# Kernel tuning notes

Hardware: AMD Instinct MI355X
Metric: run time of the kernel (lower is better)

Reference implementation:

```python
import jax, jax.numpy as jnp
import numpy as np

B, S, H = 1, 2048, 2048
I = 1408
E = 64
TOP_K = 8
N_GROUP = 8
TOPK_GROUP = 4
SCALE = 2.5
N_SHARED = 2


def setup_inputs() -> dict:
    key = jax.random.key(0)
    ks = jax.random.split(key, 9)
    x = jax.random.normal(ks[0], (B, S, H), dtype=jnp.float32)
    # kaiming_uniform(a=sqrt(5)) for [E, H] weight -> bound = 1/sqrt(H)
    gate_w = jax.random.uniform(ks[1], (E, H), jnp.float32, -1.0, 1.0) / jnp.sqrt(float(H))
    e_bias = jnp.zeros((E,), jnp.float32)
    gate_proj = jax.random.normal(ks[2], (E, I, H), jnp.float32) * 0.02
    up_proj = jax.random.normal(ks[3], (E, I, H), jnp.float32) * 0.02
    down_proj = jax.random.normal(ks[4], (E, H, I), jnp.float32) * 0.02
    SI = I * N_SHARED
    shared_gate_w = jax.random.uniform(ks[5], (SI, H), jnp.float32, -1.0, 1.0) / jnp.sqrt(float(H))
    shared_up_w = jax.random.uniform(ks[6], (SI, H), jnp.float32, -1.0, 1.0) / jnp.sqrt(float(H))
    shared_down_w = jax.random.uniform(ks[7], (H, SI), jnp.float32, -1.0, 1.0) / jnp.sqrt(float(SI))
    return {"hidden_states": x, "gate_w": gate_w, "e_bias": e_bias,
            "gate_proj": gate_proj, "up_proj": up_proj, "down_proj": down_proj,
            "shared_gate_w": shared_gate_w, "shared_up_w": shared_up_w,
            "shared_down_w": shared_down_w}


def _moe_forward(hidden_states, gate_w, e_bias, gate_proj, up_proj, down_proj,
                 shared_gate_w, shared_up_w, shared_down_w):
    bsz, seq_len, h = hidden_states.shape
    xf = hidden_states.reshape(-1, h).astype(jnp.float32)  # [T, H]
    T = bsz * seq_len

    # ---- DeepSeek group-restricted top-k gating ----
    logits = xf @ gate_w.T                                  # [T, E]
    scores = jax.nn.sigmoid(logits)
    scores_for_choice = scores + e_bias[None, :]
    gs = scores_for_choice.reshape(T, N_GROUP, E // N_GROUP)
    group_scores = jax.lax.top_k(gs, 2)[0].sum(-1)          # [T, n_group] sum of top-2 per group
    group_idx = jax.lax.top_k(group_scores, TOPK_GROUP)[1]  # [T, topk_group]
    group_mask = jax.nn.one_hot(group_idx, N_GROUP, dtype=jnp.float32).sum(1)  # [T, n_group]
    score_mask = jnp.repeat(group_mask, E // N_GROUP, axis=1)                  # [T, E]
    tmp_scores = jnp.where(score_mask > 0, scores_for_choice, 0.0)
    topk_idx = jax.lax.top_k(tmp_scores, TOP_K)[1]          # [T, top_k]
    topk_w = jnp.take_along_axis(scores, topk_idx, axis=1)  # gather from UN-biased scores
    topk_w = topk_w / (topk_w.sum(-1, keepdims=True) + 1e-20)
    topk_w = topk_w * SCALE

    # Dense combine weights [T, E]; exactly equivalent to sort/dispatch/combine.
    rows = jnp.arange(T)
    cw = jnp.zeros((T, E), jnp.float32).at[rows[:, None], topk_idx].add(topk_w)

    # ---- per-expert FFN, accumulated with lax.scan over the (fixed) expert axis ----
    def step(y, we):
        Wg, Wu, Wd, w = we                                  # [I,H],[I,H],[H,I],[T]
        g = xf @ Wg.T                                       # [T, I]
        u = xf @ Wu.T
        inter = jax.nn.silu(g) * u                          # silu_mul kernel
        out = inter @ Wd.T                                  # [T, H]
        return y + out * w[:, None], None

    y0 = jnp.zeros_like(xf)
    y, _ = jax.lax.scan(step, y0, (gate_proj, up_proj, down_proj, cw.T))
    y = y.reshape(bsz, seq_len, h)

    # ---- shared experts ----
    sg = hidden_states @ shared_gate_w.T                    # [B, S, SI]
    su = hidden_states @ shared_up_w.T
    shared_out = (jax.nn.silu(sg) * su) @ shared_down_w.T   # [B, S, H]
    return y + shared_out


def reference(hidden_states, gate_w, e_bias, gate_proj, up_proj, down_proj,
              shared_gate_w, shared_up_w, shared_down_w):
    return _moe_forward(hidden_states, gate_w, e_bias, gate_proj, up_proj, down_proj,
                        shared_gate_w, shared_up_w, shared_down_w)
```

## Files before the change

### kernel.cpp

```cpp
#include <hip/hip_runtime.h>

typedef unsigned short u16;
typedef unsigned int u32;
typedef __attribute__((ext_vector_type(8))) short short8;
typedef __attribute__((ext_vector_type(8))) u16 ushort8;
typedef __attribute__((ext_vector_type(4))) float f32x4;

#define T_TOK 2048
#define H_DIM 2048
#define NEXP 64
#define I_DIM 1408
#define SI_DIM 2816
#define BM 128
#define BK 64
#define MAXT 512

__device__ __forceinline__ u16 f2bf(float f) {
    u32 u = __builtin_bit_cast(u32, f);
    u32 r = u + 0x7FFFu + ((u >> 16) & 1u);
    return (u16)(r >> 16);
}

__device__ __forceinline__ ushort8 cvt8(f32x4 a, f32x4 b) {
    ushort8 o;
    o[0] = f2bf(a[0]); o[1] = f2bf(a[1]); o[2] = f2bf(a[2]); o[3] = f2bf(a[3]);
    o[4] = f2bf(b[0]); o[5] = f2bf(b[1]); o[6] = f2bf(b[2]); o[7] = f2bf(b[3]);
    return o;
}

__device__ __forceinline__ f32x4 mfma16(short8 a, short8 b, f32x4 c) {
    return __builtin_amdgcn_mfma_f32_16x16x32_bf16(a, b, c, 0, 0, 0);
}

__global__ __launch_bounds__(256) void k_cvt(const float* __restrict__ x, u16* __restrict__ xb) {
    int i = (blockIdx.x * 256 + threadIdx.x) * 8;
    f32x4 v0 = *(const f32x4*)(x + i);
    f32x4 v1 = *(const f32x4*)(x + i + 4);
    *(ushort8*)(xb + i) = cvt8(v0, v1);
}

__global__ __launch_bounds__(256) void k_gate_logits(const float* __restrict__ x,
        const float* __restrict__ gw, float* __restrict__ logits) {
    __shared__ float xs[8][65];
    __shared__ float wsh[64][65];
    int tid = threadIdx.x;
    int t0 = blockIdx.x * 8;
    double acc0 = 0.0, acc1 = 0.0;
    int e = tid & 63, tg = tid >> 6;
    for (int k0 = 0; k0 < H_DIM; k0 += 64) {
        #pragma unroll
        for (int s = 0; s < 2; ++s) {
            int idx = s * 256 + tid;
            int r = idx >> 6, k = idx & 63;
            xs[r][k] = x[(size_t)(t0 + r) * H_DIM + k0 + k];
        }
        #pragma unroll
        for (int s = 0; s < 16; ++s) {
            int idx = s * 256 + tid;
            int r = idx >> 6, k = idx & 63;
            wsh[r][k] = gw[(size_t)r * H_DIM + k0 + k];
        }
        __syncthreads();
        #pragma unroll 8
        for (int k = 0; k < 64; ++k) {
            double wv = (double)wsh[e][k];
            acc0 += (double)xs[tg][k] * wv;
            acc1 += (double)xs[tg + 4][k] * wv;
        }
        __syncthreads();
    }
    logits[(size_t)(t0 + tg) * NEXP + e] = (float)acc0;
    logits[(size_t)(t0 + tg + 4) * NEXP + e] = (float)acc1;
}

__global__ __launch_bounds__(256) void k_topk(const float* __restrict__ logits,
        const float* __restrict__ ebias, int* __restrict__ topk_idx,
        float* __restrict__ topk_w, int* __restrict__ counts) {
    __shared__ float bsh[64];
    if (threadIdx.x < 64) bsh[threadIdx.x] = ebias[threadIdx.x];
    __syncthreads();
    int t = blockIdx.x * 256 + threadIdx.x;
    float sc[64];
    #pragma unroll
    for (int e2 = 0; e2 < 64; ++e2) {
        float lg = logits[(size_t)t * 64 + e2];
        sc[e2] = 1.0f / (1.0f + expf(-lg));
    }
    float gsc[8];
    #pragma unroll
    for (int g = 0; g < 8; ++g) {
        float m1 = -1e30f, m2 = -1e30f;
        #pragma unroll
        for (int j = 0; j < 8; ++j) {
            float v = sc[g * 8 + j] + bsh[g * 8 + j];
            if (v > m1) { m2 = m1; m1 = v; }
            else if (v > m2) { m2 = v; }
        }
        gsc[g] = m1 + m2;
    }
    u32 gmask = 0;
    #pragma unroll
    for (int it = 0; it < 4; ++it) {
        float best = -1e30f; int bi = 0;
        #pragma unroll
        for (int g = 0; g < 8; ++g) {
            bool ok = !((gmask >> g) & 1u);
            if (ok && gsc[g] > best) { best = gsc[g]; bi = g; }
        }
        gmask |= 1u << bi;
    }
    unsigned long long avail = 0ull;
    #pragma unroll
    for (int g = 0; g < 8; ++g)
        if ((gmask >> g) & 1u) avail |= (0xFFull << (g * 8));
    float wsum = 0.f;
    int idx[8]; float wv[8];
    #pragma unroll
    for (int it = 0; it < 8; ++it) {
        float best = -1e30f, bw = 0.f; int bi = 0;
        #pragma unroll
        for (int e2 = 0; e2 < 64; ++e2) {
            bool ok = (avail >> e2) & 1ull;
            float v = sc[e2] + bsh[e2];
            if (ok && v > best) { best = v; bi = e2; bw = sc[e2]; }
        }
        avail &= ~(1ull << bi);
        idx[it] = bi; wv[it] = bw; wsum += bw;
    }
    float scale = 2.5f / (wsum + 1e-20f);
    #pragma unroll
    for (int it = 0; it < 8; ++it) {
        topk_idx[t * 8 + it] = idx[it];
        topk_w[t * 8 + it] = wv[it] * scale;
        atomicAdd(&counts[idx[it]], 1);
    }
}

__global__ void k_prefix(const int* __restrict__ counts, int* __restrict__ offsets,
                         int* __restrict__ tiles_gu, int* __restrict__ tiles_dn) {
    if (threadIdx.x == 0) {
        int run = 0;
        for (int e = 0; e < 64; ++e) { offsets[e] = run; run += counts[e]; }
        offsets[64] = run;
        for (int i = 0; i < MAXT; ++i) { tiles_gu[i] = -1; tiles_dn[i] = -1; }
        int sg[8] = {0,0,0,0,0,0,0,0};
        int sd[8] = {0,0,0,0,0,0,0,0};
        for (int j = 0; j < SI_DIM / 64; ++j) {
            int xcd = j & 7;
            int pos = xcd + 8 * sg[xcd];
            if (pos < MAXT) { tiles_gu[pos] = (64 << 16) | (j * 64); sg[xcd]++; }
        }
        for (int j = 0; j < H_DIM / 128; ++j) {
            int xcd = j & 7;
            int pos = xcd + 8 * sd[xcd];
            if (pos < MAXT) { tiles_dn[pos] = (64 << 16) | (j * 128); sd[xcd]++; }
        }
        for (int e = 0; e < 64; ++e) {
            int xcd = e & 7;
            int c = counts[e];
            for (int m0 = 0; m0 < c; m0 += BM) {
                int pg = xcd + 8 * sg[xcd];
                if (pg < MAXT) { tiles_gu[pg] = (e << 16) | m0; sg[xcd]++; }
                int pd = xcd + 8 * sd[xcd];
                if (pd < MAXT) { tiles_dn[pd] = (e << 16) | m0; sd[xcd]++; }
            }
        }
    }
}

__global__ __launch_bounds__(256) void k_scatter(const int* __restrict__ topk_idx,
        const float* __restrict__ topk_w, const int* __restrict__ offsets,
        int* __restrict__ fill, int* __restrict__ tok_list, float* __restrict__ w_list) {
    int gid = blockIdx.x * 256 + threadIdx.x;
    int t = gid >> 3;
    int e = topk_idx[gid];
    int pos = offsets[e] + atomicAdd(&fill[e], 1);
    tok_list[pos] = t;
    w_list[pos] = topk_w[gid];
}

__global__ __launch_bounds__(256, 2) void k_gateup(
        const u16* __restrict__ xb,
        const float* __restrict__ gr, const float* __restrict__ ur,
        const float* __restrict__ gs, const float* __restrict__ us,
        const int* __restrict__ offsets, const int* __restrict__ tok_list,
        const int* __restrict__ tiles,
        u16* __restrict__ inter_r, u16* __restrict__ inter_s) {
    int tt = tiles[blockIdx.x];
    if (tt < 0) return;
    int e = tt >> 16;
    const float *Bg, *Bu; u16* op; const int* tl;
    int m0, seg, n, i0, Irows;
    if (e < 64) {
        m0 = tt & 0xFFFF; seg = offsets[e]; n = offsets[e + 1] - seg;
        if (n <= 0 || m0 >= n) return;
        i0 = blockIdx.y * 64;
        Bg = gr + (size_t)e * I_DIM * H_DIM;
        Bu = ur + (size_t)e * I_DIM * H_DIM;
        op = inter_r; Irows = I_DIM; tl = tok_list;
    } else {
        if (blockIdx.y >= T_TOK / BM) return;
        i0 = tt & 0xFFFF; m0 = blockIdx.y * BM; seg = 0; n = T_TOK;
        Bg = gs; Bu = us;
        op = inter_s; Irows = SI_DIM; tl = nullptr;
    }

    __shared__ u16 As[2][BM * BK];
    __shared__ u16 Bsg[2][64 * BK];
    __shared__ u16 Bsu[2][64 * BK];

    int tid = threadIdx.x;
    int w = tid >> 6, lane = tid & 63;

    const u16* asrc[4]; int adst[4];
    #pragma unroll
    for (int s = 0; s < 4; ++s) {
        int slot = s * 256 + tid;
        int r = slot >> 3, cb = slot & 7;
        int p = m0 + r; if (p >= n) p = n - 1;
        int tok = tl ? tl[seg + p] : p;
        asrc[s] = xb + (size_t)tok * H_DIM + cb * 8;
        adst[s] = r * BK + ((cb ^ (r & 7)) * 8);
    }
    const float* bgsrc[2]; const float* busrc[2]; int bdst[2];
    #pragma unroll
    for (int s = 0; s < 2; ++s) {
        int slot = s * 256 + tid;
        int r = slot >> 3, cb = slot & 7;
        bgsrc[s] = Bg + (size_t)(i0 + r) * H_DIM + cb * 8;
        busrc[s] = Bu + (size_t)(i0 + r) * H_DIM + cb * 8;
        bdst[s] = r * BK + ((cb ^ (r & 7)) * 8);
    }

    f32x4 zero; zero[0] = 0.f; zero[1] = 0.f; zero[2] = 0.f; zero[3] = 0.f;
    f32x4 accg[2][4], accu[2][4];
    #pragma unroll
    for (int a = 0; a < 2; ++a)
        #pragma unroll
        for (int b = 0; b < 4; ++b) { accg[a][b] = zero; accu[a][b] = zero; }

    short8 stA0[4], stA1[4];
    f32x4 stG0[2][2], stU0[2][2], stG1[2][2], stU1[2][2];

    auto ldS0 = [&](int t) {
        int k0 = t * BK;
        #pragma unroll
        for (int s = 0; s < 4; ++s) stA0[s] = *(const short8*)(asrc[s] + k0);
        #pragma unroll
        for (int s = 0; s < 2; ++s) {
            stG0[s][0] = *(const f32x4*)(bgsrc[s] + k0);
            stG0[s][1] = *(const f32x4*)(bgsrc[s] + k0 + 4);
            stU0[s][0] = *(const f32x4*)(busrc[s] + k0);
            stU0[s][1] = *(const f32x4*)(busrc[s] + k0 + 4);
        }
    };
    auto ldS1 = [&](int t) {
        int k0 = t * BK;
        #pragma unroll
        for (int s = 0; s < 4; ++s) stA1[s] = *(const short8*)(asrc[s] + k0);
        #pragma unroll
        for (int s = 0; s < 2; ++s) {
            stG1[s][0] = *(const f32x4*)(bgsrc[s] + k0);
            stG1[s][1] = *(const f32x4*)(bgsrc[s] + k0 + 4);
            stU1[s][0] = *(const f32x4*)(busrc[s] + k0);
            stU1[s][1] = *(const f32x4*)(busrc[s] + k0 + 4);
        }
    };
    auto dsw0 = [&]() {
        #pragma unroll
        for (int s = 0; s < 4; ++s) *(ushort8*)(&As[0][adst[s]]) = *(const ushort8*)&stA0[s];
        #pragma unroll
        for (int s = 0; s < 2; ++s) {
            *(ushort8*)(&Bsg[0][bdst[s]]) = cvt8(stG0[s][0], stG0[s][1]);
            *(ushort8*)(&Bsu[0][bdst[s]]) = cvt8(stU0[s][0], stU0[s][1]);
        }
    };
    auto dsw1 = [&]() {
        #pragma unroll
        for (int s = 0; s < 4; ++s) *(ushort8*)(&As[1][adst[s]]) = *(const ushort8*)&stA1[s];
        #pragma unroll
        for (int s = 0; s < 2; ++s) {
            *(ushort8*)(&Bsg[1][bdst[s]]) = cvt8(stG1[s][0], stG1[s][1]);
            *(ushort8*)(&Bsu[1][bdst[s]]) = cvt8(stU1[s][0], stU1[s][1]);
        }
    };
    auto mmaStep = [&](int buf) {
        #pragma unroll
        for (int ks = 0; ks < 2; ++ks) {
            short8 a[2];
            #pragma unroll
            for (int fm = 0; fm < 2; ++fm) {
                int row = w * 32 + fm * 16 + (lane & 15);
                int cb = ks * 4 + (lane >> 4);
                a[fm] = *(const short8*)(&As[buf][row * BK + ((cb ^ (row & 7)) * 8)]);
            }
            #pragma unroll
            for (int fn = 0; fn < 4; ++fn) {
                int brow = fn * 16 + (lane & 15);
                int cb = ks * 4 + (lane >> 4);
                int boff = brow * BK + ((cb ^ (brow & 7)) * 8);
                short8 bg = *(const short8*)(&Bsg[buf][boff]);
                short8 bu = *(const short8*)(&Bsu[buf][boff]);
                accg[0][fn] = mfma16(a[0], bg, accg[0][fn]);
                accg[1][fn] = mfma16(a[1], bg, accg[1][fn]);
                accu[0][fn] = mfma16(a[0], bu, accu[0][fn]);
                accu[1][fn] = mfma16(a[1], bu, accu[1][fn]);
            }
        }
    };

    const int NK = H_DIM / BK;
    ldS0(0); dsw0();
    ldS1(1);
    __syncthreads();
    for (int t = 0; t < NK; t += 2) {
        if (t + 2 < NK) ldS0(t + 2);
        mmaStep(0);
        if (t + 1 < NK) dsw1();
        __syncthreads();
        if (t + 1 < NK) {
            if (t + 3 < NK) ldS1(t + 3);
            mmaStep(1);
            if (t + 2 < NK) dsw0();
            __syncthreads();
        }
    }

    int r0 = (lane >> 4) * 4, cc = lane & 15;
    #pragma unroll
    for (int fm = 0; fm < 2; ++fm) {
        #pragma unroll
        for (int r = 0; r < 4; ++r) {
            int p = m0 + w * 32 + fm * 16 + r0 + r;
            if (p < n) {
                size_t rowb = (size_t)(seg + p) * Irows + i0;
                #pragma unroll
                for (int fn = 0; fn < 4; ++fn) {
                    float g = accg[fm][fn][r], u = accu[fm][fn][r];
                    float val = g / (1.0f + expf(-g)) * u;
                    op[rowb + fn * 16 + cc] = f2bf(val);
                }
            }
        }
    }
}

__global__ __launch_bounds__(256, 2) void k_down(
        const u16* __restrict__ inter_r, const u16* __restrict__ inter_s,
        const float* __restrict__ dr, const float* __restrict__ dsw,
        const int* __restrict__ offsets, const int* __restrict__ tok_list,
        const int* __restrict__ tiles,
        const float* __restrict__ w_list,
        float* __restrict__ out) {
    int tt = tiles[blockIdx.x];
    if (tt < 0) return;
    int e = tt >> 16;
    const float* Bd; const u16* interp; const int* tl; const float* wl;
    int m0, seg, n, h0, Kdim;
    if (e < 64) {
        m0 = tt & 0xFFFF; seg = offsets[e]; n = offsets[e + 1] - seg;
        if (n <= 0 || m0 >= n) return;
        h0 = blockIdx.y * 128;
        Bd = dr + (size_t)e * H_DIM * I_DIM;
        interp = inter_r; Kdim = I_DIM; tl = tok_list; wl = w_list;
    } else {
        h0 = tt & 0xFFFF; m0 = blockIdx.y * BM; seg = 0; n = T_TOK;
        Bd = dsw; interp = inter_s; Kdim = SI_DIM; tl = nullptr; wl = nullptr;
    }

    __shared__ u16 As[2][BM * BK];
    __shared__ u16 Bs[2][128 * BK];

    int tid = threadIdx.x;
    int w = tid >> 6, lane = tid & 63;

    const u16* asrc[4]; int adst[4];
    #pragma unroll
    for (int s = 0; s < 4; ++s) {
        int slot = s * 256 + tid;
        int r = slot >> 3, cb = slot & 7;
        int p = m0 + r; if (p >= n) p = n - 1;
        asrc[s] = interp + (size_t)(seg + p) * Kdim + cb * 8;
        adst[s] = r * BK + ((cb ^ (r & 7)) * 8);
    }
    const float* bsrc[4]; int bdst[4];
    #pragma unroll
    for (int s = 0; s < 4; ++s) {
        int slot = s * 256 + tid;
        int r = slot >> 3, cb = slot & 7;
        bsrc[s] = Bd + (size_t)(h0 + r) * Kdim + cb * 8;
        bdst[s] = r * BK + ((cb ^ (r & 7)) * 8);
    }

    f32x4 zero; zero[0] = 0.f; zero[1] = 0.f; zero[2] = 0.f; zero[3] = 0.f;
    f32x4 acc[2][8];
    #pragma unroll
    for (int a = 0; a < 2; ++a)
        #pragma unroll
        for (int b = 0; b < 8; ++b) acc[a][b] = zero;

    short8 stA0[4], stA1[4];
    f32x4 stB0[4][2], stB1[4][2];

    auto ldS0 = [&](int t) {
        int k0 = t * BK;
        #pragma unroll
        for (int s = 0; s < 4; ++s) stA0[s] = *(const short8*)(asrc[s] + k0);
        #pragma unroll
        for (int s = 0; s < 4; ++s) {
            stB0[s][0] = *(const f32x4*)(bsrc[s] + k0);
            stB0[s][1] = *(const f32x4*)(bsrc[s] + k0 + 4);
        }
    };
    auto ldS1 = [&](int t) {
        int k0 = t * BK;
        #pragma unroll
        for (int s = 0; s < 4; ++s) stA1[s] = *(const short8*)(asrc[s] + k0);
        #pragma unroll
        for (int s = 0; s < 4; ++s) {
            stB1[s][0] = *(const f32x4*)(bsrc[s] + k0);
            stB1[s][1] = *(const f32x4*)(bsrc[s] + k0 + 4);
        }
    };
    auto dsw0 = [&]() {
        #pragma unroll
        for (int s = 0; s < 4; ++s) *(ushort8*)(&As[0][adst[s]]) = *(const ushort8*)&stA0[s];
        #pragma unroll
        for (int s = 0; s < 4; ++s)
            *(ushort8*)(&Bs[0][bdst[s]]) = cvt8(stB0[s][0], stB0[s][1]);
    };
    auto dsw1 = [&]() {
        #pragma unroll
        for (int s = 0; s < 4; ++s) *(ushort8*)(&As[1][adst[s]]) = *(const ushort8*)&stA1[s];
        #pragma unroll
        for (int s = 0; s < 4; ++s)
            *(ushort8*)(&Bs[1][bdst[s]]) = cvt8(stB1[s][0], stB1[s][1]);
    };
    auto mmaStep = [&](int buf) {
        #pragma unroll
        for (int ks = 0; ks < 2; ++ks) {
            short8 a[2];
            #pragma unroll
            for (int fm = 0; fm < 2; ++fm) {
                int row = w * 32 + fm * 16 + (lane & 15);
                int cb = ks * 4 + (lane >> 4);
                a[fm] = *(const short8*)(&As[buf][row * BK + ((cb ^ (row & 7)) * 8)]);
            }
            #pragma unroll
            for (int fn = 0; fn < 8; ++fn) {
                int brow = fn * 16 + (lane & 15);
                int cb = ks * 4 + (lane >> 4);
                short8 b = *(const short8*)(&Bs[buf][brow * BK + ((cb ^ (brow & 7)) * 8)]);
                acc[0][fn] = mfma16(a[0], b, acc[0][fn]);
                acc[1][fn] = mfma16(a[1], b, acc[1][fn]);
            }
        }
    };

    const int NK = Kdim / BK;
    ldS0(0); dsw0();
    ldS1(1);
    __syncthreads();
    for (int t = 0; t < NK; t += 2) {
        if (t + 2 < NK) ldS0(t + 2);
        mmaStep(0);
        if (t + 1 < NK) dsw1();
        __syncthreads();
        if (t + 1 < NK) {
            if (t + 3 < NK) ldS1(t + 3);
            mmaStep(1);
            if (t + 2 < NK) dsw0();
            __syncthreads();
        }
    }

    int r0 = (lane >> 4) * 4, cc = lane & 15;
    #pragma unroll
    for (int fm = 0; fm < 2; ++fm) {
        #pragma unroll
        for (int r = 0; r < 4; ++r) {
            int p = m0 + w * 32 + fm * 16 + r0 + r;
            if (p < n) {
                int tok = tl ? tl[seg + p] : p;
                float wt = wl ? wl[seg + p] : 1.0f;
                size_t ob = (size_t)tok * H_DIM + h0 + cc;
                #pragma unroll
                for (int fn = 0; fn < 8; ++fn)
                    atomicAdd(&out[ob + fn * 16], acc[fm][fn][r] * wt);
            }
        }
    }
}

extern "C" void kernel_launch(void* const* d_in, const int* in_sizes, int n_in,
                              void* d_out, int out_size, void* d_ws, size_t ws_size,
                              hipStream_t stream) {
    const float* x         = (const float*)d_in[0];
    const float* gate_w    = (const float*)d_in[1];
    const float* e_bias    = (const float*)d_in[2];
    const float* gate_proj = (const float*)d_in[3];
    const float* up_proj   = (const float*)d_in[4];
    const float* down_proj = (const float*)d_in[5];
    const float* sgw       = (const float*)d_in[6];
    const float* suw       = (const float*)d_in[7];
    const float* sdw       = (const float*)d_in[8];
    float* out = (float*)d_out;

    char* ws = (char*)d_ws;
    size_t off = 0;
    auto alloc = [&](size_t bytes) -> char* {
        char* p = ws + off;
        off += (bytes + 255) & ~(size_t)255;
        return p;
    };
    float* logits   = (float*)alloc((size_t)T_TOK * 64 * 4);
    int*   topk_idx = (int*)  alloc((size_t)T_TOK * 8 * 4);
    float* topk_w   = (float*)alloc((size_t)T_TOK * 8 * 4);
    int*   counts   = (int*)  alloc(256);
    int*   offsets  = (int*)  alloc(512);
    int*   fill     = (int*)  alloc(256);
    int*   tiles_gu = (int*)  alloc(MAXT * 4);
    int*   tiles_dn = (int*)  alloc(MAXT * 4);
    int*   tok_list = (int*)  alloc((size_t)T_TOK * 8 * 4);
    float* w_list   = (float*)alloc((size_t)T_TOK * 8 * 4);
    u16*   xb       = (u16*)  alloc((size_t)T_TOK * H_DIM * 2);
    u16*   inter_r  = (u16*)  alloc((size_t)T_TOK * 8 * I_DIM * 2);
    u16*   inter_s  = (u16*)  alloc((size_t)T_TOK * SI_DIM * 2);

    hipMemsetAsync(counts, 0, 1024, stream);
    hipMemsetAsync(out, 0, (size_t)out_size * 4, stream);

    k_cvt<<<(T_TOK * H_DIM) / 2048, 256, 0, stream>>>(x, xb);
    k_gate_logits<<<T_TOK / 8, 256, 0, stream>>>(x, gate_w, logits);
    k_topk<<<T_TOK / 256, 256, 0, stream>>>(logits, e_bias, topk_idx, topk_w, counts);
    k_prefix<<<1, 64, 0, stream>>>(counts, offsets, tiles_gu, tiles_dn);
    k_scatter<<<(T_TOK * 8) / 256, 256, 0, stream>>>(topk_idx, topk_w, offsets, fill, tok_list, w_list);

    k_gateup<<<dim3(MAXT, I_DIM / 64), 256, 0, stream>>>(
        xb, gate_proj, up_proj, sgw, suw, offsets, tok_list, tiles_gu,
        inter_r, inter_s);
    k_down<<<dim3(MAXT, H_DIM / 128), 256, 0, stream>>>(
        inter_r, inter_s, down_proj, sdw, offsets, tok_list, tiles_dn,
        w_list, out);
}
```

Baseline: 1.331 ms.

## Halve K tile to raise occupancy and replace atomic combine with gather kernel

Reduces BK from 64 to 32 with a single-stage register prefetch and a new swizzle, and raises launch bounds to 4 blocks per CU in both grouped GEMM kernels to increase occupancy. The down kernel now writes weighted routed outputs as bf16 to a per-slot buffer and writes shared-expert outputs directly, replacing float atomics on the output. A new combine kernel gathers each token's 8 slots via slot_of and adds them in. This removes atomic contention and the output memset, at the cost of extra global traffic, an extra launch, bf16 rounding of partial outputs, and more sync barriers per K step.

```diff
diff --git a/kernel.cpp b/kernel.cpp
--- a/kernel.cpp
+++ b/kernel.cpp
@@ -12,13 +12,18 @@
 #define I_DIM 1408
 #define SI_DIM 2816
 #define BM 128
-#define BK 64
+#define BK 32
 #define MAXT 512
 
 __device__ __forceinline__ u16 f2bf(float f) {
     u32 u = __builtin_bit_cast(u32, f);
     u32 r = u + 0x7FFFu + ((u >> 16) & 1u);
     return (u16)(r >> 16);
+}
+
+__device__ __forceinline__ float bf2f(u16 v) {
+    u32 u = ((u32)v) << 16;
+    return __builtin_bit_cast(float, u);
 }
 
 __device__ __forceinline__ ushort8 cvt8(f32x4 a, f32x4 b) {
@@ -30,6 +35,10 @@
 
 __device__ __forceinline__ f32x4 mfma16(short8 a, short8 b, f32x4 c) {
     return __builtin_amdgcn_mfma_f32_16x16x32_bf16(a, b, c, 0, 0, 0);
+}
+
+__device__ __forceinline__ int swz32(int r, int cb) {
+    return r * BK + ((cb ^ ((r >> 1) & 3)) * 8);
 }
 
 __global__ __launch_bounds__(256) void k_cvt(const float* __restrict__ x, u16* __restrict__ xb) {
@@ -170,16 +179,18 @@
 
 __global__ __launch_bounds__(256) void k_scatter(const int* __restrict__ topk_idx,
         const float* __restrict__ topk_w, const int* __restrict__ offsets,
-        int* __restrict__ fill, int* __restrict__ tok_list, float* __restrict__ w_list) {
+        int* __restrict__ fill, int* __restrict__ tok_list, float* __restrict__ w_list,
+        int* __restrict__ slot_of) {
     int gid = blockIdx.x * 256 + threadIdx.x;
     int t = gid >> 3;
     int e = topk_idx[gid];
     int pos = offsets[e] + atomicAdd(&fill[e], 1);
     tok_list[pos] = t;
     w_list[pos] = topk_w[gid];
-}
-
-__global__ __launch_bounds__(256, 2) void k_gateup(
+    slot_of[gid] = pos;
+}
+
+__global__ __launch_bounds__(256, 4) void k_gateup(
         const u16* __restrict__ xb,
         const float* __restrict__ gr, const float* __restrict__ ur,
         const float* __restrict__ gs, const float* __restrict__ us,
@@ -212,25 +223,20 @@
     int tid = threadIdx.x;
     int w = tid >> 6, lane = tid & 63;
 
-    const u16* asrc[4]; int adst[4];
-    #pragma unroll
-    for (int s = 0; s < 4; ++s) {
+    const u16* asrc[2]; int adst[2];
+    #pragma unroll
+    for (int s = 0; s < 2; ++s) {
         int slot = s * 256 + tid;
-        int r = slot >> 3, cb = slot & 7;
+        int r = slot >> 2, cb = slot & 3;
         int p = m0 + r; if (p >= n) p = n - 1;
         int tok = tl ? tl[seg + p] : p;
         asrc[s] = xb + (size_t)tok * H_DIM + cb * 8;
-        adst[s] = r * BK + ((cb ^ (r & 7)) * 8);
-    }
-    const float* bgsrc[2]; const float* busrc[2]; int bdst[2];
-    #pragma unroll
-    for (int s = 0; s < 2; ++s) {
-        int slot = s * 256 + tid;
-        int r = slot >> 3, cb = slot & 7;
-        bgsrc[s] = Bg + (size_t)(i0 + r) * H_DIM + cb * 8;
-        busrc[s] = Bu + (size_t)(i0 + r) * H_DIM + cb * 8;
-        bdst[s] = r * BK + ((cb ^ (r & 7)) * 8);
-    }
+        adst[s] = swz32(r, cb);
+    }
+    int br = tid >> 2, bcb = tid & 3;
+    const float* bgsrc = Bg + (size_t)(i0 + br) * H_DIM + bcb * 8;
+    const float* busrc = Bu + (size_t)(i0 + br) * H_DIM + bcb * 8;
+    int bdst = swz32(br, bcb);
 
     f32x4 zero; zero[0] = 0.f; zero[1] = 0.f; zero[2] = 0.f; zero[3] = 0.f;
     f32x4 accg[2][4], accu[2][4];
@@ -239,91 +245,54 @@
         #pragma unroll
         for (int b = 0; b < 4; ++b) { accg[a][b] = zero; accu[a][b] = zero; }
 
-    short8 stA0[4], stA1[4];
-    f32x4 stG0[2][2], stU0[2][2], stG1[2][2], stU1[2][2];
-
-    auto ldS0 = [&](int t) {
+    short8 stA[2];
+    f32x4 stG0, stG1, stU0, stU1;
+
+    auto ldregs = [&](int t) {
         int k0 = t * BK;
         #pragma unroll
-        for (int s = 0; s < 4; ++s) stA0[s] = *(const short8*)(asrc[s] + k0);
-        #pragma unroll
-        for (int s = 0; s < 2; ++s) {
-            stG0[s][0] = *(const f32x4*)(bgsrc[s] + k0);
-            stG0[s][1] = *(const f32x4*)(bgsrc[s] + k0 + 4);
-            stU0[s][0] = *(const f32x4*)(busrc[s] + k0);
-            stU0[s][1] = *(const f32x4*)(busrc[s] + k0 + 4);
-        }
-    };
-    auto ldS1 = [&](int t) {
-        int k0 = t * BK;
-        #pragma unroll
-        for (int s = 0; s < 4; ++s) stA1[s] = *(const short8*)(asrc[s] + k0);
-        #pragma unroll
-        for (int s = 0; s < 2; ++s) {
-            stG1[s][0] = *(const f32x4*)(bgsrc[s] + k0);
-            stG1[s][1] = *(const f32x4*)(bgsrc[s] + k0 + 4);
-            stU1[s][0] = *(const f32x4*)(busrc[s] + k0);
-            stU1[s][1] = *(const f32x4*)(busrc[s] + k0 + 4);
-        }
-    };
-    auto dsw0 = [&]() {
-        #pragma unroll
-        for (int s = 0; s < 4; ++s) *(ushort8*)(&As[0][adst[s]]) = *(const ushort8*)&stA0[s];
-        #pragma unroll
-        for (int s = 0; s < 2; ++s) {
-            *(ushort8*)(&Bsg[0][bdst[s]]) = cvt8(stG0[s][0], stG0[s][1]);
-            *(ushort8*)(&Bsu[0][bdst[s]]) = cvt8(stU0[s][0], stU0[s][1]);
-        }
-    };
-    auto dsw1 = [&]() {
-        #pragma unroll
-        for (int s = 0; s < 4; ++s) *(ushort8*)(&As[1][adst[s]]) = *(const ushort8*)&stA1[s];
-        #pragma unroll
-        for (int s = 0; s < 2; ++s) {
-            *(ushort8*)(&Bsg[1][bdst[s]]) = cvt8(stG1[s][0], stG1[s][1]);
-            *(ushort8*)(&Bsu[1][bdst[s]]) = cvt8(stU1[s][0], stU1[s][1]);
-        }
+        for (int s = 0; s < 2; ++s) stA[s] = *(const short8*)(asrc[s] + k0);
+        stG0 = *(const f32x4*)(bgsrc + k0);
+        stG1 = *(const f32x4*)(bgsrc + k0 + 4);
+        stU0 = *(const f32x4*)(busrc + k0);
+        stU1 = *(const f32x4*)(busrc + k0 + 4);
+    };
+    auto dswrite = [&](int buf) {
+        #pragma unroll
+        for (int s = 0; s < 2; ++s) *(ushort8*)(&As[buf][adst[s]]) = *(const ushort8*)&stA[s];
+        *(ushort8*)(&Bsg[buf][bdst]) = cvt8(stG0, stG1);
+        *(ushort8*)(&Bsu[buf][bdst]) = cvt8(stU0, stU1);
     };
     auto mmaStep = [&](int buf) {
-        #pragma unroll
-        for (int ks = 0; ks < 2; ++ks) {
-            short8 a[2];
-            #pragma unroll
-            for (int fm = 0; fm < 2; ++fm) {
-                int row = w * 32 + fm * 16 + (lane & 15);
-                int cb = ks * 4 + (lane >> 4);
-                a[fm] = *(const short8*)(&As[buf][row * BK + ((cb ^ (row & 7)) * 8)]);
-            }
-            #pragma unroll
-            for (int fn = 0; fn < 4; ++fn) {
-                int brow = fn * 16 + (lane & 15);
-                int cb = ks * 4 + (lane >> 4);
-                int boff = brow * BK + ((cb ^ (brow & 7)) * 8);
-                short8 bg = *(const short8*)(&Bsg[buf][boff]);
-                short8 bu = *(const short8*)(&Bsu[buf][boff]);
-                accg[0][fn] = mfma16(a[0], bg, accg[0][fn]);
-                accg[1][fn] = mfma16(a[1], bg, accg[1][fn]);
-                accu[0][fn] = mfma16(a[0], bu, accu[0][fn]);
-                accu[1][fn] = mfma16(a[1], bu, accu[1][fn]);
-            }
+        short8 a[2];
+        int cb = lane >> 4;
+        #pragma unroll
+        for (int fm = 0; fm < 2; ++fm) {
+            int row = w * 32 + fm * 16 + (lane & 15);
+            a[fm] = *(const short8*)(&As[buf][swz32(row, cb)]);
+        }
+        #pragma unroll
+        for (int fn = 0; fn < 4; ++fn) {
+            int brow = fn * 16 + (lane & 15);
+            int boff = swz32(brow, cb);
+            short8 bg = *(const short8*)(&Bsg[buf][boff]);
+            short8 bu = *(const short8*)(&Bsu[buf][boff]);
+            accg[0][fn] = mfma16(a[0], bg, accg[0][fn]);
+            accg[1][fn] = mfma16(a[1], bg, accg[1][fn]);
+            accu[0][fn] = mfma16(a[0], bu, accu[0][fn]);
+            accu[1][fn] = mfma16(a[1], bu, accu[1][fn]);
         }
     };
 
     const int NK = H_DIM / BK;
-    ldS0(0); dsw0();
-    ldS1(1);
+    ldregs(0);
+    dswrite(0);
     __syncthreads();
-    for (int t = 0; t < NK; t += 2) {
-        if (t + 2 < NK) ldS0(t + 2);
-        mmaStep(0);
-        if (t + 1 < NK) dsw1();
+    for (int t = 0; t < NK; ++t) {
+        if (t + 1 < NK) ldregs(t + 1);
+        mmaStep(t & 1);
+        if (t + 1 < NK) dswrite((t + 1) & 1);
         __syncthreads();
-        if (t + 1 < NK) {
-            if (t + 3 < NK) ldS1(t + 3);
-            mmaStep(1);
-            if (t + 2 < NK) dsw0();
-            __syncthreads();
-        }
     }
 
     int r0 = (lane >> 4) * 4, cc = lane & 15;
@@ -345,27 +314,27 @@
     }
 }
 
-__global__ __launch_bounds__(256, 2) void k_down(
+__global__ __launch_bounds__(256, 4) void k_down(
         const u16* __restrict__ inter_r, const u16* __restrict__ inter_s,
         const float* __restrict__ dr, const float* __restrict__ dsw,
         const int* __restrict__ offsets, const int* __restrict__ tok_list,
         const int* __restrict__ tiles,
         const float* __restrict__ w_list,
-        float* __restrict__ out) {
+        u16* __restrict__ y_r, float* __restrict__ out) {
     int tt = tiles[blockIdx.x];
     if (tt < 0) return;
     int e = tt >> 16;
-    const float* Bd; const u16* interp; const int* tl; const float* wl;
+    const float* Bd; const u16* interp; const float* wl;
     int m0, seg, n, h0, Kdim;
     if (e < 64) {
         m0 = tt & 0xFFFF; seg = offsets[e]; n = offsets[e + 1] - seg;
         if (n <= 0 || m0 >= n) return;
         h0 = blockIdx.y * 128;
         Bd = dr + (size_t)e * H_DIM * I_DIM;
-        interp = inter_r; Kdim = I_DIM; tl = tok_list; wl = w_list;
+        interp = inter_r; Kdim = I_DIM; wl = w_list;
     } else {
         h0 = tt & 0xFFFF; m0 = blockIdx.y * BM; seg = 0; n = T_TOK;
-        Bd = dsw; interp = inter_s; Kdim = SI_DIM; tl = nullptr; wl = nullptr;
+        Bd = dsw; interp = inter_s; Kdim = SI_DIM; wl = nullptr;
     }
 
     __shared__ u16 As[2][BM * BK];
@@ -374,22 +343,22 @@
     int tid = threadIdx.x;
     int w = tid >> 6, lane = tid & 63;
 
-    const u16* asrc[4]; int adst[4];
-    #pragma unroll
-    for (int s = 0; s < 4; ++s) {
+    const u16* asrc[2]; int adst[2];
+    #pragma unroll
+    for (int s = 0; s < 2; ++s) {
         int slot = s * 256 + tid;
-        int r = slot >> 3, cb = slot & 7;
+        int r = slot >> 2, cb = slot & 3;
         int p = m0 + r; if (p >= n) p = n - 1;
         asrc[s] = interp + (size_t)(seg + p) * Kdim + cb * 8;
-        adst[s] = r * BK + ((cb ^ (r & 7)) * 8);
-    }
-    const float* bsrc[4]; int bdst[4];
-    #pragma unroll
-    for (int s = 0; s < 4; ++s) {
+        adst[s] = swz32(r, cb);
+    }
+    const float* bsrc[2]; int bdst[2];
+    #pragma unroll
+    for (int s = 0; s < 2; ++s) {
         int slot = s * 256 + tid;
-        int r = slot >> 3, cb = slot & 7;
+        int r = slot >> 2, cb = slot & 3;
         bsrc[s] = Bd + (size_t)(h0 + r) * Kdim + cb * 8;
-        bdst[s] = r * BK + ((cb ^ (r & 7)) * 8);
+        bdst[s] = swz32(r, cb);
     }
 
     f32x4 zero; zero[0] = 0.f; zero[1] = 0.f; zero[2] = 0.f; zero[3] = 0.f;
@@ -399,79 +368,52 @@
         #pragma unroll
         for (int b = 0; b < 8; ++b) acc[a][b] = zero;
 
-    short8 stA0[4], stA1[4];
-    f32x4 stB0[4][2], stB1[4][2];
-
-    auto ldS0 = [&](int t) {
+    short8 stA[2];
+    f32x4 stB[2][2];
+
+    auto ldregs = [&](int t) {
         int k0 = t * BK;
         #pragma unroll
-        for (int s = 0; s < 4; ++s) stA0[s] = *(const short8*)(asrc[s] + k0);
-        #pragma unroll
-        for (int s = 0; s < 4; ++s) {
-            stB0[s][0] = *(const f32x4*)(bsrc[s] + k0);
-            stB0[s][1] = *(const f32x4*)(bsrc[s] + k0 + 4);
-        }
-    };
-    auto ldS1 = [&](int t) {
-        int k0 = t * BK;
-        #pragma unroll
-        for (int s = 0; s < 4; ++s) stA1[s] = *(const short8*)(asrc[s] + k0);
-        #pragma unroll
-        for (int s = 0; s < 4; ++s) {
-            stB1[s][0] = *(const f32x4*)(bsrc[s] + k0);
-            stB1[s][1] = *(const f32x4*)(bsrc[s] + k0 + 4);
-        }
-    };
-    auto dsw0 = [&]() {
-        #pragma unroll
-        for (int s = 0; s < 4; ++s) *(ushort8*)(&As[0][adst[s]]) = *(const ushort8*)&stA0[s];
-        #pragma unroll
-        for (int s = 0; s < 4; ++s)
-            *(ushort8*)(&Bs[0][bdst[s]]) = cvt8(stB0[s][0], stB0[s][1]);
-    };
-    auto dsw1 = [&]() {
-        #pragma unroll
-        for (int s = 0; s < 4; ++s) *(ushort8*)(&As[1][adst[s]]) = *(const ushort8*)&stA1[s];
-        #pragma unroll
-        for (int s = 0; s < 4; ++s)
-            *(ushort8*)(&Bs[1][bdst[s]]) = cvt8(stB1[s][0], stB1[s][1]);
+        for (int s = 0; s < 2; ++s) stA[s] = *(const short8*)(asrc[s] + k0);
+        #pragma unroll
+        for (int s = 0; s < 2; ++s) {
+            stB[s][0] = *(const f32x4*)(bsrc[s] + k0);
+            stB[s][1] = *(const f32x4*)(bsrc[s] + k0 + 4);
+        }
+    };
+    auto dswrite = [&](int buf) {
+        #pragma unroll
+        for (int s = 0; s < 2; ++s) *(ushort8*)(&As[buf][adst[s]]) = *(const ushort8*)&stA[s];
+        #pragma unroll
+        for (int s = 0; s < 2; ++s)
+            *(ushort8*)(&Bs[buf][bdst[s]]) = cvt8(stB[s][0], stB[s][1]);
     };
     auto mmaStep = [&](int buf) {
-        #pragma unroll
-        for (int ks = 0; ks < 2; ++ks) {
-            short8 a[2];
-            #pragma unroll
-            for (int fm = 0; fm < 2; ++fm) {
-                int row = w * 32 + fm * 16 + (lane & 15);
-                int cb = ks * 4 + (lane >> 4);
-                a[fm] = *(const short8*)(&As[buf][row * BK + ((cb ^ (row & 7)) * 8)]);
-            }
-            #pragma unroll
-            for (int fn = 0; fn < 8; ++fn) {
-                int brow = fn * 16 + (lane & 15);
-                int cb = ks * 4 + (lane >> 4);
-                short8 b = *(const short8*)(&Bs[buf][brow * BK + ((cb ^ (brow & 7)) * 8)]);
-                acc[0][fn] = mfma16(a[0], b, acc[0][fn]);
-                acc[1][fn] = mfma16(a[1], b, acc[1][fn]);
-            }
+        short8 a[2];
+        int cb = lane >> 4;
+        #pragma unroll
+        for (int fm = 0; fm < 2; ++fm) {
+            int row = w * 32 + fm * 16 + (lane & 15);
+            a[fm] = *(const short8*)(&As[buf][swz32(row, cb)]);
+        }
+        #pragma unroll
+        for (int fn = 0; fn < 8; ++fn) {
+            int brow = fn * 16 + (lane & 15);
+            short8 b = *(const short8*)(&Bs[buf][swz32(brow, cb)]);
+            acc[0][fn] = mfma16(a[0], b, acc[0][fn]);
+            acc[1][fn] = mfma16(a[1], b, acc[1][fn]);
         }
     };
 
     const int NK = Kdim / BK;
-    ldS0(0); dsw0();
-    ldS1(1);
+    ldregs(0);
+    dswrite(0);
     __syncthreads();
-    for (int t = 0; t < NK; t += 2) {
-        if (t + 2 < NK) ldS0(t + 2);
-        mmaStep(0);
-        if (t + 1 < NK) dsw1();
+    for (int t = 0; t < NK; ++t) {
+        if (t + 1 < NK) ldregs(t + 1);
+        mmaStep(t & 1);
+        if (t + 1 < NK) dswrite((t + 1) & 1);
         __syncthreads();
-        if (t + 1 < NK) {
-            if (t + 3 < NK) ldS1(t + 3);
-            mmaStep(1);
-            if (t + 2 < NK) dsw0();
-            __syncthreads();
-        }
     }
 
     int r0 = (lane >> 4) * 4, cc = lane & 15;
@@ -481,15 +423,46 @@
         for (int r = 0; r < 4; ++r) {
             int p = m0 + w * 32 + fm * 16 + r0 + r;
             if (p < n) {
-                int tok = tl ? tl[seg + p] : p;
-                float wt = wl ? wl[seg + p] : 1.0f;
-                size_t ob = (size_t)tok * H_DIM + h0 + cc;
-                #pragma unroll
-                for (int fn = 0; fn < 8; ++fn)
-                    atomicAdd(&out[ob + fn * 16], acc[fm][fn][r] * wt);
+                if (wl) {
+                    float wt = wl[seg + p];
+                    size_t ob = (size_t)(seg + p) * H_DIM + h0 + cc;
+                    #pragma unroll
+                    for (int fn = 0; fn < 8; ++fn)
+                        y_r[ob + fn * 16] = f2bf(acc[fm][fn][r] * wt);
+                } else {
+                    size_t ob = (size_t)p * H_DIM + h0 + cc;
+                    #pragma unroll
+                    for (int fn = 0; fn < 8; ++fn)
+                        out[ob + fn * 16] = acc[fm][fn][r];
+                }
             }
         }
     }
+}
+
+__global__ __launch_bounds__(256) void k_combine(const u16* __restrict__ y_r,
+        const int* __restrict__ slot_of, float* __restrict__ out) {
+    int t = blockIdx.x;
+    int c = threadIdx.x * 8;
+    int sl[8];
+    #pragma unroll
+    for (int k = 0; k < 8; ++k) sl[k] = slot_of[t * 8 + k];
+    float s[8];
+    f32x4 o0 = *(const f32x4*)(out + (size_t)t * H_DIM + c);
+    f32x4 o1 = *(const f32x4*)(out + (size_t)t * H_DIM + c + 4);
+    #pragma unroll
+    for (int j = 0; j < 4; ++j) { s[j] = o0[j]; s[4 + j] = o1[j]; }
+    #pragma unroll
+    for (int k = 0; k < 8; ++k) {
+        ushort8 v = *(const ushort8*)(y_r + (size_t)sl[k] * H_DIM + c);
+        #pragma unroll
+        for (int j = 0; j < 8; ++j) s[j] += bf2f(v[j]);
+    }
+    f32x4 r0, r1;
+    #pragma unroll
+    for (int j = 0; j < 4; ++j) { r0[j] = s[j]; r1[j] = s[4 + j]; }
+    *(f32x4*)(out + (size_t)t * H_DIM + c) = r0;
+    *(f32x4*)(out + (size_t)t * H_DIM + c + 4) = r1;
 }
 
 extern "C" void kernel_launch(void* const* d_in, const int* in_sizes, int n_in,
@@ -523,23 +496,26 @@
     int*   tiles_dn = (int*)  alloc(MAXT * 4);
     int*   tok_list = (int*)  alloc((size_t)T_TOK * 8 * 4);
     float* w_list   = (float*)alloc((size_t)T_TOK * 8 * 4);
+    int*   slot_of  = (int*)  alloc((size_t)T_TOK * 8 * 4);
     u16*   xb       = (u16*)  alloc((size_t)T_TOK * H_DIM * 2);
     u16*   inter_r  = (u16*)  alloc((size_t)T_TOK * 8 * I_DIM * 2);
     u16*   inter_s  = (u16*)  alloc((size_t)T_TOK * SI_DIM * 2);
+    u16*   y_r      = (u16*)  alloc((size_t)T_TOK * 8 * H_DIM * 2);
 
     hipMemsetAsync(counts, 0, 1024, stream);
-    hipMemsetAsync(out, 0, (size_t)out_size * 4, stream);
 
     k_cvt<<<(T_TOK * H_DIM) / 2048, 256, 0, stream>>>(x, xb);
     k_gate_logits<<<T_TOK / 8, 256, 0, stream>>>(x, gate_w, logits);
     k_topk<<<T_TOK / 256, 256, 0, stream>>>(logits, e_bias, topk_idx, topk_w, counts);
     k_prefix<<<1, 64, 0, stream>>>(counts, offsets, tiles_gu, tiles_dn);
-    k_scatter<<<(T_TOK * 8) / 256, 256, 0, stream>>>(topk_idx, topk_w, offsets, fill, tok_list, w_list);
+    k_scatter<<<(T_TOK * 8) / 256, 256, 0, stream>>>(topk_idx, topk_w, offsets, fill,
+                                                     tok_list, w_list, slot_of);
 
     k_gateup<<<dim3(MAXT, I_DIM / 64), 256, 0, stream>>>(
         xb, gate_proj, up_proj, sgw, suw, offsets, tok_list, tiles_gu,
         inter_r, inter_s);
     k_down<<<dim3(MAXT, H_DIM / 128), 256, 0, stream>>>(
         inter_r, inter_s, down_proj, sdw, offsets, tok_list, tiles_dn,
-        w_list, out);
-}
+        w_list, y_r, out);
+    k_combine<<<T_TOK, 256, 0, stream>>>(y_r, slot_of, out);
+}
```

Result: slower. 1.565 ms (+17.6%).

## Replace atomic scatter-add in down GEMM with bf16 staging and combine kernel

Applied to the files above, without the earlier changes.

The down-projection kernel no longer scatters weighted results into the output with fp32 atomics. Routed expert outputs are written as bf16 rows into a per-slot buffer, the shared-expert result is stored directly into the output, and a new combine kernel sums the eight routed slots per token. A slot_of map from the scatter kernel locates each token's slots. This removes atomic contention and the output memset, but adds a 64MB intermediate write and read, one more launch, and bf16 rounding of the routed partial outputs.

```diff
diff --git a/kernel.cpp b/kernel.cpp
--- a/kernel.cpp
+++ b/kernel.cpp
@@ -19,6 +19,11 @@
     u32 u = __builtin_bit_cast(u32, f);
     u32 r = u + 0x7FFFu + ((u >> 16) & 1u);
     return (u16)(r >> 16);
+}
+
+__device__ __forceinline__ float bf2f(u16 v) {
+    u32 u = ((u32)v) << 16;
+    return __builtin_bit_cast(float, u);
 }
 
 __device__ __forceinline__ ushort8 cvt8(f32x4 a, f32x4 b) {
@@ -170,13 +175,15 @@
 
 __global__ __launch_bounds__(256) void k_scatter(const int* __restrict__ topk_idx,
         const float* __restrict__ topk_w, const int* __restrict__ offsets,
-        int* __restrict__ fill, int* __restrict__ tok_list, float* __restrict__ w_list) {
+        int* __restrict__ fill, int* __restrict__ tok_list, float* __restrict__ w_list,
+        int* __restrict__ slot_of) {
     int gid = blockIdx.x * 256 + threadIdx.x;
     int t = gid >> 3;
     int e = topk_idx[gid];
     int pos = offsets[e] + atomicAdd(&fill[e], 1);
     tok_list[pos] = t;
     w_list[pos] = topk_w[gid];
+    slot_of[gid] = pos;
 }
 
 __global__ __launch_bounds__(256, 2) void k_gateup(
@@ -351,21 +358,21 @@
         const int* __restrict__ offsets, const int* __restrict__ tok_list,
         const int* __restrict__ tiles,
         const float* __restrict__ w_list,
-        float* __restrict__ out) {
+        u16* __restrict__ y_r, float* __restrict__ out) {
     int tt = tiles[blockIdx.x];
     if (tt < 0) return;
     int e = tt >> 16;
-    const float* Bd; const u16* interp; const int* tl; const float* wl;
+    const float* Bd; const u16* interp; const float* wl;
     int m0, seg, n, h0, Kdim;
     if (e < 64) {
         m0 = tt & 0xFFFF; seg = offsets[e]; n = offsets[e + 1] - seg;
         if (n <= 0 || m0 >= n) return;
         h0 = blockIdx.y * 128;
         Bd = dr + (size_t)e * H_DIM * I_DIM;
-        interp = inter_r; Kdim = I_DIM; tl = tok_list; wl = w_list;
+        interp = inter_r; Kdim = I_DIM; wl = w_list;
     } else {
         h0 = tt & 0xFFFF; m0 = blockIdx.y * BM; seg = 0; n = T_TOK;
-        Bd = dsw; interp = inter_s; Kdim = SI_DIM; tl = nullptr; wl = nullptr;
+        Bd = dsw; interp = inter_s; Kdim = SI_DIM; wl = nullptr;
     }
 
     __shared__ u16 As[2][BM * BK];
@@ -481,15 +488,46 @@
         for (int r = 0; r < 4; ++r) {
             int p = m0 + w * 32 + fm * 16 + r0 + r;
             if (p < n) {
-                int tok = tl ? tl[seg + p] : p;
-                float wt = wl ? wl[seg + p] : 1.0f;
-                size_t ob = (size_t)tok * H_DIM + h0 + cc;
-                #pragma unroll
-                for (int fn = 0; fn < 8; ++fn)
-                    atomicAdd(&out[ob + fn * 16], acc[fm][fn][r] * wt);
-            }
-        }
-    }
+                if (wl) {
+                    float wt = wl[seg + p];
+                    size_t ob = (size_t)(seg + p) * H_DIM + h0 + cc;
+                    #pragma unroll
+                    for (int fn = 0; fn < 8; ++fn)
+                        y_r[ob + fn * 16] = f2bf(acc[fm][fn][r] * wt);
+                } else {
+                    size_t ob = (size_t)p * H_DIM + h0 + cc;
+                    #pragma unroll
+                    for (int fn = 0; fn < 8; ++fn)
+                        out[ob + fn * 16] = acc[fm][fn][r];
+                }
+            }
+        }
+    }
+}
+
+__global__ __launch_bounds__(256) void k_combine(const u16* __restrict__ y_r,
+        const int* __restrict__ slot_of, float* __restrict__ out) {
+    int t = blockIdx.x;
+    int c = threadIdx.x * 8;
+    int sl[8];
+    #pragma unroll
+    for (int k = 0; k < 8; ++k) sl[k] = slot_of[t * 8 + k];
+    float s[8];
+    f32x4 o0 = *(const f32x4*)(out + (size_t)t * H_DIM + c);
+    f32x4 o1 = *(const f32x4*)(out + (size_t)t * H_DIM + c + 4);
+    #pragma unroll
+    for (int j = 0; j < 4; ++j) { s[j] = o0[j]; s[4 + j] = o1[j]; }
+    #pragma unroll
+    for (int k = 0; k < 8; ++k) {
+        ushort8 v = *(const ushort8*)(y_r + (size_t)sl[k] * H_DIM + c);
+        #pragma unroll
+        for (int j = 0; j < 8; ++j) s[j] += bf2f(v[j]);
+    }
+    f32x4 r0, r1;
+    #pragma unroll
+    for (int j = 0; j < 4; ++j) { r0[j] = s[j]; r1[j] = s[4 + j]; }
+    *(f32x4*)(out + (size_t)t * H_DIM + c) = r0;
+    *(f32x4*)(out + (size_t)t * H_DIM + c + 4) = r1;
 }
 
 extern "C" void kernel_launch(void* const* d_in, const int* in_sizes, int n_in,
@@ -523,23 +561,26 @@
     int*   tiles_dn = (int*)  alloc(MAXT * 4);
     int*   tok_list = (int*)  alloc((size_t)T_TOK * 8 * 4);
     float* w_list   = (float*)alloc((size_t)T_TOK * 8 * 4);
+    int*   slot_of  = (int*)  alloc((size_t)T_TOK * 8 * 4);
     u16*   xb       = (u16*)  alloc((size_t)T_TOK * H_DIM * 2);
     u16*   inter_r  = (u16*)  alloc((size_t)T_TOK * 8 * I_DIM * 2);
     u16*   inter_s  = (u16*)  alloc((size_t)T_TOK * SI_DIM * 2);
+    u16*   y_r      = (u16*)  alloc((size_t)T_TOK * 8 * H_DIM * 2);
 
     hipMemsetAsync(counts, 0, 1024, stream);
-    hipMemsetAsync(out, 0, (size_t)out_size * 4, stream);
 
     k_cvt<<<(T_TOK * H_DIM) / 2048, 256, 0, stream>>>(x, xb);
     k_gate_logits<<<T_TOK / 8, 256, 0, stream>>>(x, gate_w, logits);
     k_topk<<<T_TOK / 256, 256, 0, stream>>>(logits, e_bias, topk_idx, topk_w, counts);
     k_prefix<<<1, 64, 0, stream>>>(counts, offsets, tiles_gu, tiles_dn);
-    k_scatter<<<(T_TOK * 8) / 256, 256, 0, stream>>>(topk_idx, topk_w, offsets, fill, tok_list, w_list);
+    k_scatter<<<(T_TOK * 8) / 256, 256, 0, stream>>>(topk_idx, topk_w, offsets, fill,
+                                                     tok_list, w_list, slot_of);
 
     k_gateup<<<dim3(MAXT, I_DIM / 64), 256, 0, stream>>>(
         xb, gate_proj, up_proj, sgw, suw, offsets, tok_list, tiles_gu,
         inter_r, inter_s);
     k_down<<<dim3(MAXT, H_DIM / 128), 256, 0, stream>>>(
         inter_r, inter_s, down_proj, sdw, offsets, tok_list, tiles_dn,
-        w_list, out);
-}
+        w_list, y_r, out);
+    k_combine<<<T_TOK, 256, 0, stream>>>(y_r, slot_of, out);
+}
```

Measured after the change: 1.308 ms. About the same (-1.7%).
